# Performance work log

Measured on AMD Instinct MI355X. Metric: run time of the kernel, lower is better.

Reference implementation:

```python
import jax, jax.numpy as jnp
import numpy as np

# --- static config (matches init_kwargs) ---
DEPTH, HEADS, DIM, EMBED, TXT_DIM = 4, 16, 1024, 768, 4096
T, GH, GW, N_TEXT = 8, 14, 14, 16          # temporal blocks, grid H, grid W, text tokens
HD = DIM // HEADS                          # head dim = 64
SCALE = HD ** -0.5
MLP_H = int(4.0 * DIM)
F_TOK = T * GH * GW                        # frame tokens = 1568


def _ln(x, w, b, eps=1e-5):
    m = jnp.mean(x, axis=-1, keepdims=True)
    v = jnp.var(x, axis=-1, keepdims=True)
    return (x - m) * jax.lax.rsqrt(v + eps) * w + b


def _rope_cos_sin():
    # 3D axial RoPE over (frame, height, width); per-axis rotary dim d=2*((HD//3)//2)=20.
    d = 2 * ((HD // 3) // 2)
    ids = jnp.arange(F_TOK)
    hw = GH * GW
    pos = jnp.stack([ids // hw, (ids % hw) // GW, ids % GW], 0).astype(jnp.float32)  # [3,F]
    omega = jnp.arange(d // 2, dtype=jnp.float32) / (d / 2.0)
    inv = 1.0 / (10000.0 ** omega)                       # [d/2]
    freq = pos[:, :, None] * inv                          # [3,F,d/2]
    freq = jnp.repeat(freq, 2, axis=-1)                   # interleaved pairs -> [3,F,d]
    freq = jnp.concatenate([freq[0], freq[1], freq[2]], -1)  # [F, 3d]
    freq = jnp.pad(freq, ((0, 0), (0, HD - 3 * d)))       # remainder dims: identity rotation
    freq = jnp.pad(freq, ((N_TEXT, 0), (0, 0)))           # text tokens: identity rotation
    return jnp.cos(freq), jnp.sin(freq)                   # each [N, HD]


def _rot_pairs(x):
    # (x0,x1) -> (-x1,x0) on interleaved pairs
    x2 = x.reshape(x.shape[:-1] + (HD // 2, 2))
    return jnp.stack([-x2[..., 1], x2[..., 0]], -1).reshape(x.shape)


def _mask_bias():
    # text-text: causal tril; frame->text: full; frame-frame: block-causal by frame id
    N = N_TEXT + F_TOK
    m = np.zeros((N, N), dtype=bool)
    m[:N_TEXT, :N_TEXT] = np.tril(np.ones((N_TEXT, N_TEXT), dtype=bool))
    m[N_TEXT:, :N_TEXT] = True
    fid = np.arange(F_TOK) // (GH * GW)
    m[N_TEXT:, N_TEXT:] = fid[None, :] <= fid[:, None]
    return jnp.where(jnp.asarray(m), 0.0, -1e9).astype(jnp.float32)


def _block(x, p, cos, sin, bias):
    (ln1_w, ln1_b, qkv_w, qkv_b, proj_w, proj_b,
     ln2_w, ln2_b, fc1_w, fc1_b, fc2_w, fc2_b) = p
    B, N, _ = x.shape
    h = _ln(x, ln1_w, ln1_b)
    qkv = (h @ qkv_w + qkv_b).reshape(B, N, 3, HEADS, HD).transpose(2, 0, 3, 1, 4)
    q, k, v = qkv[0], qkv[1], qkv[2]                      # [B,H,N,HD]
    q = q * cos + _rot_pairs(q) * sin
    k = k * cos + _rot_pairs(k) * sin
    att = jnp.einsum("bhqd,bhkd->bhqk", q, k) * SCALE + bias
    att = jax.nn.softmax(att, axis=-1)
    o = jnp.einsum("bhqk,bhkd->bhqd", att, v).transpose(0, 2, 1, 3).reshape(B, N, DIM)
    x = x + o @ proj_w + proj_b
    h = _ln(x, ln2_w, ln2_b)
    h = jax.nn.gelu(h @ fc1_w + fc1_b, approximate=False)
    return x + h @ fc2_w + fc2_b


def setup_inputs() -> dict:
    key = jax.random.key(0)
    ks = jax.random.split(key, 10)
    std = 0.02
    W = lambda k, s: jax.random.normal(k, s, jnp.float32) * std
    inp = {
        "x": jax.random.normal(ks[0], (1, F_TOK, EMBED), jnp.float32),
        "text_instruction": jax.random.normal(ks[1], (1, N_TEXT, TXT_DIM), jnp.float32),
        "w_embed": W(ks[2], (EMBED, DIM)), "b_embed": jnp.zeros((DIM,), jnp.float32),
        "w_text": W(ks[3], (TXT_DIM, DIM)), "b_text": jnp.zeros((DIM,), jnp.float32),
        "ln1_w": jnp.ones((DEPTH, DIM), jnp.float32), "ln1_b": jnp.zeros((DEPTH, DIM), jnp.float32),
        "qkv_w": W(ks[4], (DEPTH, DIM, 3 * DIM)), "qkv_b": jnp.zeros((DEPTH, 3 * DIM), jnp.float32),
        "proj_w": W(ks[5], (DEPTH, DIM, DIM)), "proj_b": jnp.zeros((DEPTH, DIM), jnp.float32),
        "ln2_w": jnp.ones((DEPTH, DIM), jnp.float32), "ln2_b": jnp.zeros((DEPTH, DIM), jnp.float32),
        "fc1_w": W(ks[6], (DEPTH, DIM, MLP_H)), "fc1_b": jnp.zeros((DEPTH, MLP_H), jnp.float32),
        "fc2_w": W(ks[7], (DEPTH, MLP_H, DIM)), "fc2_b": jnp.zeros((DEPTH, DIM), jnp.float32),
        "normf_w": jnp.ones((DIM,), jnp.float32), "normf_b": jnp.zeros((DIM,), jnp.float32),
        "w_out": W(ks[8], (DIM, EMBED)), "b_out": jnp.zeros((EMBED,), jnp.float32),
    }
    # _rescale_blocks: proj and fc2 weights divided by sqrt(2*layer_id)
    sc = 1.0 / jnp.sqrt(2.0 * (jnp.arange(DEPTH, dtype=jnp.float32) + 1.0))
    inp["proj_w"] = inp["proj_w"] * sc[:, None, None]
    inp["fc2_w"] = inp["fc2_w"] * sc[:, None, None]
    return inp


def reference(x, text_instruction, w_embed, b_embed, w_text, b_text,
              ln1_w, ln1_b, qkv_w, qkv_b, proj_w, proj_b,
              ln2_w, ln2_b, fc1_w, fc1_b, fc2_w, fc2_b,
              normf_w, normf_b, w_out, b_out):
    h = x @ w_embed + b_embed                      # predictor_embed
    t = text_instruction @ w_text + b_text         # text_encoder
    h = jnp.concatenate([t, h], axis=1)            # [B, N_TEXT + F_TOK, DIM]
    cos, sin = _rope_cos_sin()
    bias = _mask_bias()
    params = (ln1_w, ln1_b, qkv_w, qkv_b, proj_w, proj_b,
              ln2_w, ln2_b, fc1_w, fc1_b, fc2_w, fc2_b)
    def step(carry, p):
        return _block(carry, p, cos, sin, bias), None
    h, _ = jax.lax.scan(step, h, params)
    h = h[:, N_TEXT:, :]                           # drop text tokens
    h = _ln(h, normf_w, normf_b)
    return h @ w_out + b_out                       # predictor_proj -> [B, F_TOK, EMBED]
```

## Files before the change

### kernel.cpp

```cpp
#include <hip/hip_runtime.h>
#include <hip/hip_bf16.h>
#include <math.h>

#define HEADS 16
#define DIM 1024
#define N_TEXT 16
#define F_TOK 1568
#define NTOK 1584
#define MPAD 1664
#define SCALEF 0.125f

typedef unsigned int uint;
typedef unsigned short u16;

typedef __bf16 bf16x8 __attribute__((ext_vector_type(8)));
typedef float f32x4 __attribute__((ext_vector_type(4)));

__device__ inline u16 f2b(float f){
  uint u = __builtin_bit_cast(uint, f);
  uint r = u + 0x7fffu + ((u >> 16) & 1u);
  return (u16)(r >> 16);
}

__device__ inline f32x4 mfma16(bf16x8 a, bf16x8 b, f32x4 c){
  return __builtin_amdgcn_mfma_f32_16x16x32_bf16(a, b, c, 0, 0, 0);
}

__device__ __forceinline__ void gload16(const u16* g, u16* l){
  __builtin_amdgcn_global_load_lds(
      (__attribute__((address_space(1))) u16*)const_cast<u16*>(g),
      (__attribute__((address_space(3))) u16*)l, 16, 0, 0);
}

__global__ __launch_bounds__(256) void wtrans_kernel(const float* __restrict__ src,
                                                     u16* __restrict__ dst, int K, int N){
  __shared__ float tile[32][33];
  int n0 = blockIdx.x * 32, k0 = blockIdx.y * 32;
  int t = threadIdx.x;
  int col = t & 31, rb = t >> 5;
#pragma unroll
  for (int p = 0; p < 4; ++p){
    int row = p*8 + rb;
    tile[row][col] = src[(size_t)(k0+row)*N + n0 + col];
  }
  __syncthreads();
#pragma unroll
  for (int p = 0; p < 4; ++p){
    int rn = p*8 + rb;
    dst[(size_t)(n0+rn)*K + k0 + col] = f2b(tile[col][rn]);
  }
}

__global__ __launch_bounds__(256) void f2b_kernel(const float* __restrict__ src,
                                                  u16* __restrict__ dst, int n){
  int i = blockIdx.x*256 + threadIdx.x;
  if (i < n) dst[i] = f2b(src[i]);
}

__global__ __launch_bounds__(256) void rope_table_kernel(float* __restrict__ ct,
                                                         float* __restrict__ st){
  int i = blockIdx.x*256 + threadIdx.x;
  if (i >= NTOK*64) return;
  int n = i >> 6, d = i & 63;
  float f = 0.f;
  if (n >= N_TEXT){
    int id = n - N_TEXT;
    int p0 = id / 196;
    int p1 = (id % 196) / 14;
    int p2 = id % 14;
    float pos = 0.f; int j = -1;
    if (d < 20){ pos = (float)p0; j = d >> 1; }
    else if (d < 40){ pos = (float)p1; j = (d-20) >> 1; }
    else if (d < 60){ pos = (float)p2; j = (d-40) >> 1; }
    if (j >= 0){
      float inv = powf(10000.f, -(float)j * 0.1f);
      f = pos * inv;
    }
  }
  ct[i] = cosf(f);
  st[i] = sinf(f);
}

__global__ __launch_bounds__(256) void rope_apply_kernel(const float* __restrict__ qkv,
    const float* __restrict__ ct, const float* __restrict__ st,
    u16* __restrict__ qb, u16* __restrict__ kb, u16* __restrict__ vb){
  int i = blockIdx.x*256 + threadIdx.x;
  if (i >= NTOK*HEADS*32) return;
  int n = i / 512;
  int rem = i & 511;
  int h = rem >> 5;
  int d0 = (rem & 31) * 2;
  size_t base = (size_t)n*3072 + h*64 + d0;
  float q0 = qkv[base],      q1 = qkv[base+1];
  float k0 = qkv[base+1024], k1 = qkv[base+1025];
  float v0 = qkv[base+2048], v1 = qkv[base+2049];
  float c = ct[n*64+d0], s = st[n*64+d0];
  size_t ob = ((size_t)h*MPAD + n)*64 + d0;
  qb[ob]   = f2b(q0*c - q1*s);
  qb[ob+1] = f2b(q1*c + q0*s);
  kb[ob]   = f2b(k0*c - k1*s);
  kb[ob+1] = f2b(k1*c + k0*s);
  vb[ob]   = f2b(v0);
  vb[ob+1] = f2b(v1);
}

__global__ __launch_bounds__(256) void ln_kernel(const float* __restrict__ x,
    const float* __restrict__ w, const float* __restrict__ b, u16* __restrict__ out){
  int row = blockIdx.x, t = threadIdx.x;
  const float* xr = x + (size_t)row * DIM;
  float4 v = *(const float4*)&xr[t*4];
  float s = v.x+v.y+v.z+v.w;
  float ss = v.x*v.x+v.y*v.y+v.z*v.z+v.w*v.w;
#pragma unroll
  for (int o=32;o>0;o>>=1){ s += __shfl_down(s,o,64); ss += __shfl_down(ss,o,64); }
  __shared__ float red[8];
  int wid = t>>6;
  if ((t&63)==0){ red[wid] = s; red[4+wid] = ss; }
  __syncthreads();
  float S = red[0]+red[1]+red[2]+red[3];
  float SS = red[4]+red[5]+red[6]+red[7];
  float mean = S * (1.0f/1024.0f);
  float var = SS * (1.0f/1024.0f) - mean*mean;
  float inv = rsqrtf(var + 1e-5f);
  ushort4 o4;
  o4.x = f2b((v.x-mean)*inv*w[t*4+0]+b[t*4+0]);
  o4.y = f2b((v.y-mean)*inv*w[t*4+1]+b[t*4+1]);
  o4.z = f2b((v.z-mean)*inv*w[t*4+2]+b[t*4+2]);
  o4.w = f2b((v.w-mean)*inv*w[t*4+3]+b[t*4+3]);
  *(ushort4*)&out[(size_t)row*DIM + t*4] = o4;
}

template<int EPI>
__global__ __launch_bounds__(256, 2)
void gemm2_kernel(const u16* __restrict__ A, const u16* __restrict__ BT,
                  const float* __restrict__ bias,
                  float* __restrict__ outF, u16* __restrict__ outB,
                  int M, int N, int K, int klen, size_t partStride)
{
  __shared__ u16 L[2][2][128*64];
  const int t = threadIdx.x, wid = t >> 6, lane = t & 63;
  const int lr = lane & 15, lg = lane >> 4;
  const int wr = wid >> 1, wc = wid & 1;
  const int m0 = blockIdx.y * 128, n0 = blockIdx.x * 128;
  const int kstart = blockIdx.z * klen;

  const int srow = lane >> 3;
  const int scol = ((lane & 7) ^ srow) * 8;
  const u16* Ast = A  + (size_t)(m0 + srow)*K + kstart + scol;
  const u16* Bst = BT + (size_t)(n0 + srow)*K + kstart + scol;

  const int s0 = (lg     ) ^ (lr & 7);
  const int s1 = (lg + 4 ) ^ (lr & 7);
  const int aBase = (wr*64 + lr)*64;
  const int bBase = (wc*64 + lr)*64;

  f32x4 acc[4][4] = {};
  const int nk = klen >> 6;

  auto STAGE = [&](int buf, int step){
    const u16* a = Ast + (size_t)step*64;
    const u16* b = Bst + (size_t)step*64;
#pragma unroll
    for (int j = 0; j < 4; ++j){
      int c = wid*4 + j;
      gload16(a + (size_t)c*8*K, &L[buf][0][c*512]);
      gload16(b + (size_t)c*8*K, &L[buf][1][c*512]);
    }
  };

  STAGE(0, 0);
  __syncthreads();
  int cur = 0;
  for (int tt = 0; tt < nk; ++tt){
    if (tt + 1 < nk) STAGE(cur ^ 1, tt + 1);
    const u16* Ab = &L[cur][0][0];
    const u16* Bb = &L[cur][1][0];
    bf16x8 af[2][4], bv[2][4];
#pragma unroll
    for (int m = 0; m < 4; ++m){
      af[0][m] = *(const bf16x8*)&Ab[aBase + m*1024 + s0*8];
      af[1][m] = *(const bf16x8*)&Ab[aBase + m*1024 + s1*8];
    }
#pragma unroll
    for (int n = 0; n < 4; ++n){
      bv[0][n] = *(const bf16x8*)&Bb[bBase + n*1024 + s0*8];
      bv[1][n] = *(const bf16x8*)&Bb[bBase + n*1024 + s1*8];
    }
#pragma unroll
    for (int ks = 0; ks < 2; ++ks)
#pragma unroll
      for (int m = 0; m < 4; ++m)
#pragma unroll
        for (int n = 0; n < 4; ++n)
          acc[m][n] = mfma16(af[ks][m], bv[ks][n], acc[m][n]);
    __syncthreads();
    cur ^= 1;
  }

#pragma unroll
  for (int m = 0; m < 4; ++m){
#pragma unroll
    for (int r = 0; r < 4; ++r){
      int row = m0 + wr*64 + m*16 + lg*4 + r;
      if (row >= M) continue;
#pragma unroll
      for (int n = 0; n < 4; ++n){
        int col = n0 + wc*64 + n*16 + lr;
        float v = acc[m][n][r];
        if constexpr (EPI == 4){
          outF[partStride*blockIdx.z + (size_t)row*N + col] = v;
        } else if constexpr (EPI == 3){
          v += bias[col];
          v = 0.5f * v * (1.0f + erff(v * 0.70710678118654752f));
          outB[(size_t)row*N + col] = f2b(v);
        } else {
          v += bias[col];
          outF[(size_t)row*N + col] = v;
        }
      }
    }
  }
}

__global__ __launch_bounds__(256) void reduce_kernel(const float* __restrict__ part,
    size_t stride, int S, const float* __restrict__ bias, const float* __restrict__ resid,
    float* __restrict__ out, int MN, int N){
  int i = (blockIdx.x*256 + threadIdx.x)*4;
  if (i >= MN) return;
  float4 v = *(const float4*)&bias[i % N];
  if (resid){
    float4 r = *(const float4*)&resid[i];
    v.x += r.x; v.y += r.y; v.z += r.z; v.w += r.w;
  }
  for (int s = 0; s < S; ++s){
    float4 p = *(const float4*)&part[(size_t)s*stride + i];
    v.x += p.x; v.y += p.y; v.z += p.z; v.w += p.w;
  }
  *(float4*)&out[i] = v;
}

__device__ inline float bias_fn(int qi, int ki){
  if (ki >= NTOK) return -1e9f;
  if (qi < N_TEXT) return (ki <= qi) ? 0.f : -1e9f;
  if (ki < N_TEXT) return 0.f;
  int fq = (qi - N_TEXT) / 196;
  int fk = (ki - N_TEXT) / 196;
  return (fk <= fq) ? 0.f : -1e9f;
}

__global__ __launch_bounds__(256)
void attn_kernel(const u16* __restrict__ qb, const u16* __restrict__ kb,
                 const u16* __restrict__ vb, u16* __restrict__ ob)
{
  __shared__ u16 Kl[64][72];
  __shared__ u16 Vl[64][72];
  __shared__ u16 Pl[128][72];
  const int hh = blockIdx.y;
  const int q0 = blockIdx.x * 128;
  const int t = threadIdx.x, wid = t>>6, lane = t&63, lr = lane&15, lg = lane>>4;

  bf16x8 qf[2][2];
#pragma unroll
  for (int m=0;m<2;++m)
#pragma unroll
    for (int ks=0;ks<2;++ks){
      int row = q0 + wid*32 + m*16 + lr;
      qf[m][ks] = *(const bf16x8*)&qb[((size_t)hh*MPAD + row)*64 + ks*32 + lg*8];
    }

  float mrun[8], lrun[8];
#pragma unroll
  for (int i=0;i<8;++i){ mrun[i] = -3.0e38f; lrun[i] = 0.0f; }
  f32x4 oacc[2][4] = {};

  for (int kbi = 0; kbi < 25; ++kbi){
    int k0 = kbi*64;
#pragma unroll
    for (int p=0;p<2;++p){
      int sidx = t + p*256;
      int row = sidx >> 3, c8 = (sidx & 7) * 8;
      *(uint4*)&Kl[row][c8] = *(const uint4*)&kb[((size_t)hh*MPAD + k0 + row)*64 + c8];
    }
#pragma unroll
    for (int p=0;p<2;++p){
      int sidx = t + p*256;
      int kk = sidx & 63, d8 = (sidx >> 6) * 8;
      union { uint4 u; u16 s[8]; } tv;
      tv.u = *(const uint4*)&vb[((size_t)hh*MPAD + k0 + kk)*64 + d8];
#pragma unroll
      for (int j=0;j<8;++j) Vl[d8+j][kk] = tv.s[j];
    }
    __syncthreads();

    f32x4 sacc[2][4] = {};
#pragma unroll
    for (int n=0;n<4;++n){
      bf16x8 kf0 = *(const bf16x8*)&Kl[n*16 + lr][lg*8];
      bf16x8 kf1 = *(const bf16x8*)&Kl[n*16 + lr][32 + lg*8];
#pragma unroll
      for (int m=0;m<2;++m){
        sacc[m][n] = mfma16(qf[m][0], kf0, sacc[m][n]);
        sacc[m][n] = mfma16(qf[m][1], kf1, sacc[m][n]);
      }
    }

    float sval[2][4][4];
    float pmax[8];
#pragma unroll
    for (int i=0;i<8;++i) pmax[i] = -3.0e38f;
#pragma unroll
    for (int m=0;m<2;++m)
#pragma unroll
      for (int n=0;n<4;++n)
#pragma unroll
        for (int r=0;r<4;++r){
          int qi = q0 + wid*32 + m*16 + lg*4 + r;
          int ki = k0 + n*16 + lr;
          float v = sacc[m][n][r]*SCALEF + bias_fn(qi, ki);
          sval[m][n][r] = v;
          pmax[m*4+r] = fmaxf(pmax[m*4+r], v);
        }
#pragma unroll
    for (int i=0;i<8;++i){
      float v = pmax[i];
      v = fmaxf(v, __shfl_xor(v,1,64));
      v = fmaxf(v, __shfl_xor(v,2,64));
      v = fmaxf(v, __shfl_xor(v,4,64));
      v = fmaxf(v, __shfl_xor(v,8,64));
      pmax[i] = v;
    }
    float alpha[8], psum[8];
#pragma unroll
    for (int i=0;i<8;++i){
      float mnew = fmaxf(mrun[i], pmax[i]);
      alpha[i] = expf(mrun[i] - mnew);
      mrun[i] = mnew;
      psum[i] = 0.f;
    }
#pragma unroll
    for (int m=0;m<2;++m)
#pragma unroll
      for (int r=0;r<4;++r){
        float mn = mrun[m*4+r];
#pragma unroll
        for (int n=0;n<4;++n){
          float p = expf(sval[m][n][r] - mn);
          psum[m*4+r] += p;
          Pl[wid*32 + m*16 + lg*4 + r][n*16 + lr] = f2b(p);
        }
      }
#pragma unroll
    for (int i=0;i<8;++i){
      float v = psum[i];
      v += __shfl_xor(v,1,64); v += __shfl_xor(v,2,64);
      v += __shfl_xor(v,4,64); v += __shfl_xor(v,8,64);
      lrun[i] = lrun[i]*alpha[i] + v;
    }
#pragma unroll
    for (int m=0;m<2;++m)
#pragma unroll
      for (int n=0;n<4;++n)
#pragma unroll
        for (int r=0;r<4;++r)
          oacc[m][n][r] *= alpha[m*4+r];
    __syncthreads();

#pragma unroll
    for (int m=0;m<2;++m){
      bf16x8 pf0 = *(const bf16x8*)&Pl[wid*32 + m*16 + lr][lg*8];
      bf16x8 pf1 = *(const bf16x8*)&Pl[wid*32 + m*16 + lr][32 + lg*8];
#pragma unroll
      for (int n=0;n<4;++n){
        bf16x8 vf0 = *(const bf16x8*)&Vl[n*16 + lr][lg*8];
        bf16x8 vf1 = *(const bf16x8*)&Vl[n*16 + lr][32 + lg*8];
        oacc[m][n] = mfma16(pf0, vf0, oacc[m][n]);
        oacc[m][n] = mfma16(pf1, vf1, oacc[m][n]);
      }
    }
    __syncthreads();
  }

#pragma unroll
  for (int m=0;m<2;++m)
#pragma unroll
    for (int n=0;n<4;++n)
#pragma unroll
      for (int r=0;r<4;++r){
        int row = q0 + wid*32 + m*16 + lg*4 + r;
        int col = hh*64 + n*16 + lr;
        float v = oacc[m][n][r] / lrun[m*4+r];
        ob[(size_t)row*DIM + col] = f2b(v);
      }
}

extern "C" void kernel_launch(void* const* d_in, const int* in_sizes, int n_in,
                              void* d_out, int out_size, void* d_ws, size_t ws_size,
                              hipStream_t stream)
{
  const float* x       = (const float*)d_in[0];
  const float* text    = (const float*)d_in[1];
  const float* w_embed = (const float*)d_in[2];
  const float* b_embed = (const float*)d_in[3];
  const float* w_text  = (const float*)d_in[4];
  const float* b_text  = (const float*)d_in[5];
  const float* ln1_w   = (const float*)d_in[6];
  const float* ln1_b   = (const float*)d_in[7];
  const float* qkv_w   = (const float*)d_in[8];
  const float* qkv_b   = (const float*)d_in[9];
  const float* proj_w  = (const float*)d_in[10];
  const float* proj_b  = (const float*)d_in[11];
  const float* ln2_w   = (const float*)d_in[12];
  const float* ln2_b   = (const float*)d_in[13];
  const float* fc1_w   = (const float*)d_in[14];
  const float* fc1_b   = (const float*)d_in[15];
  const float* fc2_w   = (const float*)d_in[16];
  const float* fc2_b   = (const float*)d_in[17];
  const float* normf_w = (const float*)d_in[18];
  const float* normf_b = (const float*)d_in[19];
  const float* w_out   = (const float*)d_in[20];
  const float* b_out   = (const float*)d_in[21];
  (void)in_sizes; (void)n_in; (void)out_size;

  char* ws = (char*)d_ws;
  size_t off = 0;
  auto alloc = [&](size_t bytes)->void*{
    void* p = ws + off; off += (bytes + 255) & ~(size_t)255; return p;
  };
  u16* wTe  = (u16*)alloc((size_t)1024*768*2);
  u16* wTt  = (u16*)alloc((size_t)1024*4096*2);
  u16* wTq  = (u16*)alloc((size_t)4*3072*1024*2);
  u16* wTp  = (u16*)alloc((size_t)4*1024*1024*2);
  u16* wT1  = (u16*)alloc((size_t)4*4096*1024*2);
  u16* wT2  = (u16*)alloc((size_t)4*1024*4096*2);
  u16* wTo  = (u16*)alloc((size_t)768*1024*2);
  u16* xbf  = (u16*)alloc((size_t)MPAD*768*2);
  u16* tbf  = (u16*)alloc((size_t)128*4096*2);
  float* h  = (float*)alloc((size_t)MPAD*1024*4);
  u16* lno  = (u16*)alloc((size_t)MPAD*1024*2);
  float* qkv= (float*)alloc((size_t)MPAD*3072*4);
  u16* qbuf = (u16*)alloc((size_t)HEADS*MPAD*64*2);
  u16* kbuf = (u16*)alloc((size_t)HEADS*MPAD*64*2);
  u16* vbuf = (u16*)alloc((size_t)HEADS*MPAD*64*2);
  u16* obf  = (u16*)alloc((size_t)MPAD*1024*2);
  u16* mlp  = (u16*)alloc((size_t)MPAD*4096*2);
  float* ct = (float*)alloc((size_t)NTOK*64*4);
  float* st = (float*)alloc((size_t)NTOK*64*4);
  float* partF = (float*)alloc((size_t)4*MPAD*1024*4);
  if (off > ws_size) return;
  float* projPart = (float*)mlp;

  wtrans_kernel<<<dim3(1024/32, 768/32), 256, 0, stream>>>(w_embed, wTe, 768, 1024);
  wtrans_kernel<<<dim3(1024/32, 4096/32), 256, 0, stream>>>(w_text, wTt, 4096, 1024);
  for (int l=0;l<4;++l){
    wtrans_kernel<<<dim3(3072/32, 1024/32),256,0,stream>>>(qkv_w + (size_t)l*1024*3072, wTq + (size_t)l*3072*1024, 1024, 3072);
    wtrans_kernel<<<dim3(1024/32, 1024/32),256,0,stream>>>(proj_w + (size_t)l*1024*1024, wTp + (size_t)l*1024*1024, 1024, 1024);
    wtrans_kernel<<<dim3(4096/32, 1024/32),256,0,stream>>>(fc1_w + (size_t)l*1024*4096, wT1 + (size_t)l*4096*1024, 1024, 4096);
    wtrans_kernel<<<dim3(1024/32, 4096/32),256,0,stream>>>(fc2_w + (size_t)l*4096*1024, wT2 + (size_t)l*1024*4096, 4096, 1024);
  }
  wtrans_kernel<<<dim3(768/32, 1024/32),256,0,stream>>>(w_out, wTo, 1024, 768);

  f2b_kernel<<<(F_TOK*768+255)/256,256,0,stream>>>(x, xbf, F_TOK*768);
  f2b_kernel<<<(16*4096+255)/256,256,0,stream>>>(text, tbf, 16*4096);
  rope_table_kernel<<<(NTOK*64+255)/256,256,0,stream>>>(ct, st);

  gemm2_kernel<4><<<dim3(8,1,8),256,0,stream>>>(tbf, wTt, nullptr, partF, nullptr,
      16, 1024, 4096, 512, (size_t)16*1024);
  reduce_kernel<<<(16*1024/4+255)/256,256,0,stream>>>(partF, (size_t)16*1024, 8, b_text, nullptr, h, 16*1024, 1024);
  gemm2_kernel<0><<<dim3(8,13,1),256,0,stream>>>(xbf, wTe, b_embed, h + (size_t)16*1024, nullptr,
      1568, 1024, 768, 768, 0);

  for (int l=0;l<4;++l){
    ln_kernel<<<MPAD,256,0,stream>>>(h, ln1_w + l*1024, ln1_b + l*1024, lno);
    gemm2_kernel<0><<<dim3(24,13,1),256,0,stream>>>(lno, wTq + (size_t)l*3072*1024, qkv_b + l*3072,
        qkv, nullptr, MPAD, 3072, 1024, 1024, 0);
    rope_apply_kernel<<<(NTOK*512+255)/256,256,0,stream>>>(qkv, ct, st, qbuf, kbuf, vbuf);
    attn_kernel<<<dim3(13,16),256,0,stream>>>(qbuf, kbuf, vbuf, obf);
    gemm2_kernel<4><<<dim3(8,13,2),256,0,stream>>>(obf, wTp + (size_t)l*1024*1024, nullptr,
        projPart, nullptr, MPAD, 1024, 1024, 512, (size_t)MPAD*1024);
    reduce_kernel<<<(MPAD*1024/4+255)/256,256,0,stream>>>(projPart, (size_t)MPAD*1024, 2,
        proj_b + l*1024, h, h, MPAD*1024, 1024);
    ln_kernel<<<MPAD,256,0,stream>>>(h, ln2_w + l*1024, ln2_b + l*1024, lno);
    gemm2_kernel<3><<<dim3(32,13,1),256,0,stream>>>(lno, wT1 + (size_t)l*4096*1024, fc1_b + l*4096,
        nullptr, mlp, MPAD, 4096, 1024, 1024, 0);
    gemm2_kernel<4><<<dim3(8,13,4),256,0,stream>>>(mlp, wT2 + (size_t)l*1024*4096, nullptr,
        partF, nullptr, MPAD, 1024, 4096, 1024, (size_t)MPAD*1024);
    reduce_kernel<<<(MPAD*1024/4+255)/256,256,0,stream>>>(partF, (size_t)MPAD*1024, 4,
        fc2_b + l*1024, h, h, MPAD*1024, 1024);
  }

  ln_kernel<<<F_TOK,256,0,stream>>>(h + (size_t)16*1024, normf_w, normf_b, lno);
  gemm2_kernel<4><<<dim3(6,13,4),256,0,stream>>>(lno, wTo, nullptr, partF, nullptr,
      F_TOK, 768, 1024, 256, (size_t)F_TOK*768);
  reduce_kernel<<<(F_TOK*768/4+255)/256,256,0,stream>>>(partF, (size_t)F_TOK*768, 4,
      b_out, nullptr, (float*)d_out, F_TOK*768, 768);
}
```

Baseline: 1.180 ms.

## Skip fully masked key tiles in attention and halve query tile size

The attention kernel now works out, for each 64-row query tile, the last key position any of its rows can see under the block-causal mask, and loops only over key tiles up to that point instead of all 25. The query tile shrinks from 128 to 64 rows, so there are twice as many workgroups (26x16), which spreads the uneven per-tile work more evenly across CUs. The per-element bias function is replaced by a precomputed per-row limit compare, and expf becomes __expf. In exchange, K/V tiles are reloaded from memory by twice as many blocks, and the fast exp is less precise.

New measurement: 1.067 ms. 9.6% less time.

```diff
diff --git a/kernel.cpp b/kernel.cpp
--- a/kernel.cpp
+++ b/kernel.cpp
@@ -239,158 +239,143 @@
   *(float4*)&out[i] = v;
 }
 
-__device__ inline float bias_fn(int qi, int ki){
-  if (ki >= NTOK) return -1e9f;
-  if (qi < N_TEXT) return (ki <= qi) ? 0.f : -1e9f;
-  if (ki < N_TEXT) return 0.f;
-  int fq = (qi - N_TEXT) / 196;
-  int fk = (ki - N_TEXT) / 196;
-  return (fk <= fq) ? 0.f : -1e9f;
-}
-
 __global__ __launch_bounds__(256)
 void attn_kernel(const u16* __restrict__ qb, const u16* __restrict__ kb,
                  const u16* __restrict__ vb, u16* __restrict__ ob)
 {
   __shared__ u16 Kl[64][72];
   __shared__ u16 Vl[64][72];
-  __shared__ u16 Pl[128][72];
+  __shared__ u16 Pl[64][72];
   const int hh = blockIdx.y;
-  const int q0 = blockIdx.x * 128;
+  const int q0 = blockIdx.x * 64;
   const int t = threadIdx.x, wid = t>>6, lane = t&63, lr = lane&15, lg = lane>>4;
-
-  bf16x8 qf[2][2];
-#pragma unroll
-  for (int m=0;m<2;++m)
-#pragma unroll
-    for (int ks=0;ks<2;++ks){
-      int row = q0 + wid*32 + m*16 + lr;
-      qf[m][ks] = *(const bf16x8*)&qb[((size_t)hh*MPAD + row)*64 + ks*32 + lg*8];
-    }
-
-  float mrun[8], lrun[8];
-#pragma unroll
-  for (int i=0;i<8;++i){ mrun[i] = -3.0e38f; lrun[i] = 0.0f; }
-  f32x4 oacc[2][4] = {};
-
-  for (int kbi = 0; kbi < 25; ++kbi){
-    int k0 = kbi*64;
+  const size_t hbase = (size_t)hh*MPAD*64;
+
+  bf16x8 qf[2];
+  {
+    int row = q0 + wid*16 + lr;
+    qf[0] = *(const bf16x8*)&qb[hbase + (size_t)row*64 + lg*8];
+    qf[1] = *(const bf16x8*)&qb[hbase + (size_t)row*64 + 32 + lg*8];
+  }
+
+  int lim[4];
+#pragma unroll
+  for (int r=0;r<4;++r){
+    int qi = q0 + wid*16 + lg*4 + r;
+    int L = (qi < N_TEXT) ? (qi + 1) : (16 + ((qi - 16)/196 + 1)*196);
+    lim[r] = min(L, NTOK);
+  }
+  const int qlast = min(q0 + 63, NTOK - 1);
+  const int kend  = (qlast < N_TEXT) ? (qlast + 1)
+                                     : min(16 + ((qlast - 16)/196 + 1)*196, NTOK);
+  const int nkt = (kend + 63) >> 6;
+
+  float mrun[4], lrun[4];
+#pragma unroll
+  for (int i=0;i<4;++i){ mrun[i] = -3.0e38f; lrun[i] = 0.0f; }
+  f32x4 oacc[4] = {};
+
+  for (int kbi = 0; kbi < nkt; ++kbi){
+    const int k0 = kbi*64;
 #pragma unroll
     for (int p=0;p<2;++p){
       int sidx = t + p*256;
       int row = sidx >> 3, c8 = (sidx & 7) * 8;
-      *(uint4*)&Kl[row][c8] = *(const uint4*)&kb[((size_t)hh*MPAD + k0 + row)*64 + c8];
+      *(uint4*)&Kl[row][c8] = *(const uint4*)&kb[hbase + (size_t)(k0 + row)*64 + c8];
     }
 #pragma unroll
     for (int p=0;p<2;++p){
       int sidx = t + p*256;
       int kk = sidx & 63, d8 = (sidx >> 6) * 8;
       union { uint4 u; u16 s[8]; } tv;
-      tv.u = *(const uint4*)&vb[((size_t)hh*MPAD + k0 + kk)*64 + d8];
+      tv.u = *(const uint4*)&vb[hbase + (size_t)(k0 + kk)*64 + d8];
 #pragma unroll
       for (int j=0;j<8;++j) Vl[d8+j][kk] = tv.s[j];
     }
     __syncthreads();
 
-    f32x4 sacc[2][4] = {};
+    f32x4 sacc[4] = {};
 #pragma unroll
     for (int n=0;n<4;++n){
       bf16x8 kf0 = *(const bf16x8*)&Kl[n*16 + lr][lg*8];
       bf16x8 kf1 = *(const bf16x8*)&Kl[n*16 + lr][32 + lg*8];
-#pragma unroll
-      for (int m=0;m<2;++m){
-        sacc[m][n] = mfma16(qf[m][0], kf0, sacc[m][n]);
-        sacc[m][n] = mfma16(qf[m][1], kf1, sacc[m][n]);
+      sacc[n] = mfma16(qf[0], kf0, sacc[n]);
+      sacc[n] = mfma16(qf[1], kf1, sacc[n]);
+    }
+
+    float sval[4][4];
+    float pmax[4] = {-3.0e38f, -3.0e38f, -3.0e38f, -3.0e38f};
+#pragma unroll
+    for (int n=0;n<4;++n){
+      int ki = k0 + n*16 + lr;
+#pragma unroll
+      for (int r=0;r<4;++r){
+        float v = (ki < lim[r]) ? sacc[n][r]*SCALEF : -3.0e38f;
+        sval[n][r] = v;
+        pmax[r] = fmaxf(pmax[r], v);
       }
     }
-
-    float sval[2][4][4];
-    float pmax[8];
-#pragma unroll
-    for (int i=0;i<8;++i) pmax[i] = -3.0e38f;
-#pragma unroll
-    for (int m=0;m<2;++m)
-#pragma unroll
-      for (int n=0;n<4;++n)
-#pragma unroll
-        for (int r=0;r<4;++r){
-          int qi = q0 + wid*32 + m*16 + lg*4 + r;
-          int ki = k0 + n*16 + lr;
-          float v = sacc[m][n][r]*SCALEF + bias_fn(qi, ki);
-          sval[m][n][r] = v;
-          pmax[m*4+r] = fmaxf(pmax[m*4+r], v);
-        }
-#pragma unroll
-    for (int i=0;i<8;++i){
-      float v = pmax[i];
+#pragma unroll
+    for (int r=0;r<4;++r){
+      float v = pmax[r];
       v = fmaxf(v, __shfl_xor(v,1,64));
       v = fmaxf(v, __shfl_xor(v,2,64));
       v = fmaxf(v, __shfl_xor(v,4,64));
       v = fmaxf(v, __shfl_xor(v,8,64));
-      pmax[i] = v;
-    }
-    float alpha[8], psum[8];
-#pragma unroll
-    for (int i=0;i<8;++i){
-      float mnew = fmaxf(mrun[i], pmax[i]);
-      alpha[i] = expf(mrun[i] - mnew);
-      mrun[i] = mnew;
-      psum[i] = 0.f;
-    }
-#pragma unroll
-    for (int m=0;m<2;++m)
-#pragma unroll
-      for (int r=0;r<4;++r){
-        float mn = mrun[m*4+r];
-#pragma unroll
-        for (int n=0;n<4;++n){
-          float p = expf(sval[m][n][r] - mn);
-          psum[m*4+r] += p;
-          Pl[wid*32 + m*16 + lg*4 + r][n*16 + lr] = f2b(p);
-        }
+      pmax[r] = v;
+    }
+    float alpha[4], psum[4];
+#pragma unroll
+    for (int r=0;r<4;++r){
+      float mnew = fmaxf(mrun[r], pmax[r]);
+      alpha[r] = __expf(mrun[r] - mnew);
+      mrun[r] = mnew;
+      psum[r] = 0.f;
+    }
+#pragma unroll
+    for (int r=0;r<4;++r){
+      float mn = mrun[r];
+#pragma unroll
+      for (int n=0;n<4;++n){
+        float p = __expf(sval[n][r] - mn);
+        psum[r] += p;
+        Pl[wid*16 + lg*4 + r][n*16 + lr] = f2b(p);
       }
-#pragma unroll
-    for (int i=0;i<8;++i){
-      float v = psum[i];
+    }
+#pragma unroll
+    for (int r=0;r<4;++r){
+      float v = psum[r];
       v += __shfl_xor(v,1,64); v += __shfl_xor(v,2,64);
       v += __shfl_xor(v,4,64); v += __shfl_xor(v,8,64);
-      lrun[i] = lrun[i]*alpha[i] + v;
-    }
-#pragma unroll
-    for (int m=0;m<2;++m)
-#pragma unroll
-      for (int n=0;n<4;++n)
-#pragma unroll
-        for (int r=0;r<4;++r)
-          oacc[m][n][r] *= alpha[m*4+r];
+      lrun[r] = lrun[r]*alpha[r] + v;
+    }
+#pragma unroll
+    for (int n=0;n<4;++n)
+#pragma unroll
+      for (int r=0;r<4;++r)
+        oacc[n][r] *= alpha[r];
     __syncthreads();
 
-#pragma unroll
-    for (int m=0;m<2;++m){
-      bf16x8 pf0 = *(const bf16x8*)&Pl[wid*32 + m*16 + lr][lg*8];
-      bf16x8 pf1 = *(const bf16x8*)&Pl[wid*32 + m*16 + lr][32 + lg*8];
-#pragma unroll
-      for (int n=0;n<4;++n){
-        bf16x8 vf0 = *(const bf16x8*)&Vl[n*16 + lr][lg*8];
-        bf16x8 vf1 = *(const bf16x8*)&Vl[n*16 + lr][32 + lg*8];
-        oacc[m][n] = mfma16(pf0, vf0, oacc[m][n]);
-        oacc[m][n] = mfma16(pf1, vf1, oacc[m][n]);
-      }
+    bf16x8 pf0 = *(const bf16x8*)&Pl[wid*16 + lr][lg*8];
+    bf16x8 pf1 = *(const bf16x8*)&Pl[wid*16 + lr][32 + lg*8];
+#pragma unroll
+    for (int n=0;n<4;++n){
+      bf16x8 vf0 = *(const bf16x8*)&Vl[n*16 + lr][lg*8];
+      bf16x8 vf1 = *(const bf16x8*)&Vl[n*16 + lr][32 + lg*8];
+      oacc[n] = mfma16(pf0, vf0, oacc[n]);
+      oacc[n] = mfma16(pf1, vf1, oacc[n]);
     }
     __syncthreads();
   }
 
 #pragma unroll
-  for (int m=0;m<2;++m)
-#pragma unroll
-    for (int n=0;n<4;++n)
-#pragma unroll
-      for (int r=0;r<4;++r){
-        int row = q0 + wid*32 + m*16 + lg*4 + r;
-        int col = hh*64 + n*16 + lr;
-        float v = oacc[m][n][r] / lrun[m*4+r];
-        ob[(size_t)row*DIM + col] = f2b(v);
-      }
+  for (int n=0;n<4;++n)
+#pragma unroll
+    for (int r=0;r<4;++r){
+      int row = q0 + wid*16 + lg*4 + r;
+      int col = hh*64 + n*16 + lr;
+      ob[(size_t)row*DIM + col] = f2b(oacc[n][r] / lrun[r]);
+    }
 }
 
 extern "C" void kernel_launch(void* const* d_in, const int* in_sizes, int n_in,
@@ -474,7 +459,7 @@
     gemm2_kernel<0><<<dim3(24,13,1),256,0,stream>>>(lno, wTq + (size_t)l*3072*1024, qkv_b + l*3072,
         qkv, nullptr, MPAD, 3072, 1024, 1024, 0);
     rope_apply_kernel<<<(NTOK*512+255)/256,256,0,stream>>>(qkv, ct, st, qbuf, kbuf, vbuf);
-    attn_kernel<<<dim3(13,16),256,0,stream>>>(qbuf, kbuf, vbuf, obf);
+    attn_kernel<<<dim3(MPAD/64,16),256,0,stream>>>(qbuf, kbuf, vbuf, obf);
     gemm2_kernel<4><<<dim3(8,13,2),256,0,stream>>>(obf, wTp + (size_t)l*1024*1024, nullptr,
         projPart, nullptr, MPAD, 1024, 1024, 512, (size_t)MPAD*1024);
     reduce_kernel<<<(MPAD*1024/4+255)/256,256,0,stream>>>(projPart, (size_t)MPAD*1024, 2,
```
